# Kernel optimization log

Hardware: AMD Instinct MI355X
Metric: run time of the kernel (lower is better)

Reference implementation:

```python
import jax, jax.numpy as jnp
import numpy as np


def setup_inputs() -> dict:
    key = jax.random.key(0)
    ks = jax.random.split(key, 4)
    B, H, W, C = 4, 64, 64, 256
    d = C // 8
    x = jax.random.normal(ks[0], (B, H, W, C), dtype=jnp.float32)
    # 1x1 conv weights as [C_in, C_out] matrices (Glorot-ish scale)
    Wq = jax.random.normal(ks[1], (C, d), dtype=jnp.float32) * (1.0 / np.sqrt(C))
    Wk = jax.random.normal(ks[2], (C, d), dtype=jnp.float32) * (1.0 / np.sqrt(C))
    Wv = jax.random.normal(ks[3], (C, C), dtype=jnp.float32) * (1.0 / np.sqrt(C))
    bq = jnp.zeros((d,), dtype=jnp.float32)
    bk = jnp.zeros((d,), dtype=jnp.float32)
    bv = jnp.zeros((C,), dtype=jnp.float32)
    gamma = jnp.float32(0.0)  # matches tf.Variable(0.0)
    return {"x": x, "Wq": Wq, "bq": bq, "Wk": Wk, "bk": bk, "Wv": Wv, "bv": bv, "gamma": gamma}


def reference(x, Wq, bq, Wk, bk, Wv, bv, gamma):
    B, H, W, C = x.shape
    N = H * W
    xf = x.reshape(B, N, C)  # spatial tokens
    q = xf @ Wq + bq  # [B, N, d]
    k = xf @ Wk + bk  # [B, N, d]
    v = xf @ Wv + bv  # [B, N, C]
    energy = jnp.einsum("bnd,bmd->bnm", q, k)  # [B, N, N]
    attn = jax.nn.softmax(energy, axis=-1)
    out = jnp.einsum("bnm,bmc->bnc", attn, v).reshape(B, H, W, C)
    return gamma * out + x
```

## Files before the change

kernel.cpp:

```cpp
#include <hip/hip_runtime.h>
#include <hip/hip_bf16.h>

typedef __attribute__((ext_vector_type(8)))  short short8;
typedef __attribute__((ext_vector_type(4)))  float f32x4;
typedef __attribute__((ext_vector_type(16))) float f32x16;
typedef __attribute__((ext_vector_type(4)))  unsigned int u32x4;

#define LOG2E 1.4426950408889634f

static __device__ __forceinline__ unsigned short f2bf(float f) {
    union { float f; unsigned u; } v; v.f = f;
    unsigned r = v.u + 0x7fffu + ((v.u >> 16) & 1u);
    return (unsigned short)(r >> 16);
}
static __device__ __forceinline__ unsigned cvt_pk_bf16(float lo, float hi) {
    unsigned r;
    asm("v_cvt_pk_bf16_f32 %0, %1, %2" : "=v"(r) : "v"(lo), "v"(hi));
    return r;
}
static __device__ __forceinline__ float exp2_hw(float x) {
    float r;
    asm("v_exp_f32 %0, %1" : "=v"(r) : "v"(x));
    return r;
}

__global__ __launch_bounds__(64) void transpose_w(
    const float* __restrict__ Wq, const float* __restrict__ Wk,
    const float* __restrict__ Wv, unsigned short* __restrict__ Wtf)
{
    const int g  = blockIdx.x;
    const int ct = g >> 3, kk = g & 7;
    const int l  = threadIdx.x;
    const int col = ct * 16 + (l & 15);
    const int k0  = kk * 32 + (l >> 4) * 8;
    const float* W; int c, ldw;
    if (col < 32)      { W = Wq; c = col;      ldw = 32;  }
    else if (col < 64) { W = Wk; c = col - 32; ldw = 32;  }
    else               { W = Wv; c = col - 64; ldw = 256; }
    ushort4 o0, o1;
    o0.x = f2bf(W[(size_t)(k0 + 0) * ldw + c]);
    o0.y = f2bf(W[(size_t)(k0 + 1) * ldw + c]);
    o0.z = f2bf(W[(size_t)(k0 + 2) * ldw + c]);
    o0.w = f2bf(W[(size_t)(k0 + 3) * ldw + c]);
    o1.x = f2bf(W[(size_t)(k0 + 4) * ldw + c]);
    o1.y = f2bf(W[(size_t)(k0 + 5) * ldw + c]);
    o1.z = f2bf(W[(size_t)(k0 + 6) * ldw + c]);
    o1.w = f2bf(W[(size_t)(k0 + 7) * ldw + c]);
    *reinterpret_cast<ushort4*>(Wtf + (size_t)g * 512 + l * 8)     = o0;
    *reinterpret_cast<ushort4*>(Wtf + (size_t)g * 512 + l * 8 + 4) = o1;
}

__global__ __launch_bounds__(256) void proj_kernel(
    const float* __restrict__ x, const unsigned short* __restrict__ Wtf,
    const float* __restrict__ bq, const float* __restrict__ bk,
    const float* __restrict__ bv,
    unsigned short* __restrict__ Qb, unsigned short* __restrict__ Kf,
    unsigned short* __restrict__ Vf)
{
    __shared__ unsigned short x_lds[64][264];
    const int tid = threadIdx.x;
    const int M0  = (blockIdx.x >> 1) * 64;
    const int ctb = (blockIdx.x & 1) * 10;

    #pragma unroll
    for (int j = 0; j < 16; ++j) {
        int idx = j * 256 + tid;
        int row = idx >> 6;
        int qc  = idx & 63;
        const float4 v = *reinterpret_cast<const float4*>(x + (size_t)(M0 + row) * 256 + qc * 4);
        ushort4 o;
        o.x = f2bf(v.x); o.y = f2bf(v.y); o.z = f2bf(v.z); o.w = f2bf(v.w);
        *reinterpret_cast<ushort4*>(&x_lds[row][qc * 4]) = o;
    }
    __syncthreads();

    const int w  = tid >> 6;
    const int l  = tid & 63;
    const int lr = l & 15;
    const int lg = l >> 4;

    short8 a[8];
    #pragma unroll
    for (int kk = 0; kk < 8; ++kk)
        a[kk] = *reinterpret_cast<const short8*>(&x_lds[w * 16 + lr][kk * 32 + lg * 8]);

    const int b   = M0 >> 12;
    const int kt  = (M0 & 4095) >> 6;

    for (int ct = ctb; ct < ctb + 10; ++ct) {
        const int col = ct * 16 + lr;
        f32x4 acc = {0.f, 0.f, 0.f, 0.f};
        #pragma unroll
        for (int kk = 0; kk < 8; ++kk) {
            const short8 bfr = *reinterpret_cast<const short8*>(
                Wtf + ((size_t)ct * 8 + kk) * 512 + l * 8);
            acc = __builtin_amdgcn_mfma_f32_16x16x32_bf16(a[kk], bfr, acc, 0, 0, 0);
        }
        const int rbase = M0 + w * 16 + lg * 4;
        if (ct < 2) {
            const float bias = bq[col];
            #pragma unroll
            for (int r = 0; r < 4; ++r)
                Qb[(size_t)(rbase + r) * 32 + col] = f2bf((acc[r] + bias) * LOG2E);
        } else if (ct < 4) {
            const int colp = col - 32;
            const float bias = bk[colp];
            const int dd = colp >> 4, hj = (colp >> 3) & 1, jj = colp & 7;
            #pragma unroll
            for (int r = 0; r < 4; ++r) {
                const int tt = (rbase + r) & 4095;
                const size_t e = (size_t)b * 131072 + (size_t)kt * 2048
                               + (((tt >> 5) & 1) * 2 + dd) * 512
                               + (hj * 32 + (tt & 31)) * 8 + jj;
                Kf[e] = f2bf(acc[r] + bias);
            }
        } else {
            const int colp = col - 64;
            const float bias = bv[colp];
            const int kk_f = w;
            const int hi_v = (lg >> 1) & 1;
            const int j0   = (lg & 1) * 4;
            const size_t e = (size_t)b * 1048576 + (size_t)kt * 16384
                           + (colp >> 5) * 2048 + kk_f * 512
                           + (hi_v * 32 + (colp & 31)) * 8 + j0;
            ushort4 o;
            o.x = f2bf(acc[0] + bias); o.y = f2bf(acc[1] + bias);
            o.z = f2bf(acc[2] + bias); o.w = f2bf(acc[3] + bias);
            *reinterpret_cast<ushort4*>(Vf + e) = o;
        }
    }
}

__global__ __launch_bounds__(512, 2) void attn_kernel(
    const unsigned short* __restrict__ Qb, const unsigned short* __restrict__ Kf,
    const unsigned short* __restrict__ Vf, const float* __restrict__ x,
    const float* __restrict__ gamma_p, float* __restrict__ out)
{
    __shared__ float Obuf[2][32][260];
    __shared__ float lbuf[2][4][32];

    const int i  = blockIdx.x;
    const int b  = i & 3;
    const int qt = i >> 2;

    const int tid = threadIdx.x;
    const int w   = tid >> 6;
    const int qs  = w & 1;
    const int kh  = w >> 1;
    const int l   = tid & 63;
    const int l5  = l & 31;
    const int hi  = l >> 5;

    const size_t bN = (size_t)b * 4096;
    const int q0 = qt * 64;

    const unsigned short* Kfb = Kf + (size_t)b * 131072 + l * 8;
    const unsigned short* Vfb = Vf + (size_t)b * 1048576 + l * 8;

    short8 qb[2];
    #pragma unroll
    for (int dd = 0; dd < 2; ++dd)
        qb[dd] = *reinterpret_cast<const short8*>(
            Qb + (bN + (size_t)(q0 + qs * 32 + l5)) * 32 + dd * 16 + hi * 8);

    f32x16 Oa[8];
    #pragma unroll
    for (int ct = 0; ct < 8; ++ct)
        #pragma unroll
        for (int r = 0; r < 16; ++r) Oa[ct][r] = 0.f;
    float lsum0 = 0.f, lsum1 = 0.f;

    f32x16 z;
    #pragma unroll
    for (int r = 0; r < 16; ++r) z[r] = 0.f;

    const int kt0 = kh * 16;

    auto loadK = [&](short8 (&kA)[2][2], int ktg) {
        const unsigned short* kp = Kfb + (size_t)ktg * 2048;
        #pragma unroll
        for (int ks = 0; ks < 2; ++ks)
            #pragma unroll
            for (int dd = 0; dd < 2; ++dd)
                kA[ks][dd] = *reinterpret_cast<const short8*>(kp + (ks * 2 + dd) * 512);
    };

    short8 pa[4];
    auto build_pa = [&](const f32x16& p, int base) {
        float e[16];
        #pragma unroll
        for (int r = 0; r < 16; ++r) {
            e[r] = exp2_hw(p[r]);
            if (r & 1) lsum1 += e[r]; else lsum0 += e[r];
        }
        unsigned c[8];
        #pragma unroll
        for (int n = 0; n < 8; ++n) c[n] = cvt_pk_bf16(e[2 * n], e[2 * n + 1]);
        #pragma unroll
        for (int k2 = 0; k2 < 2; ++k2) {
            unsigned d0 = c[4 * k2 + 0], d2 = c[4 * k2 + 2];
            unsigned d1 = c[4 * k2 + 1], d3 = c[4 * k2 + 3];
            asm("v_permlane32_swap_b32 %0, %1" : "+v"(d0), "+v"(d2));
            asm("v_permlane32_swap_b32 %0, %1" : "+v"(d1), "+v"(d3));
            u32x4 u = {d0, d1, d2, d3};
            pa[base + k2] = __builtin_bit_cast(short8, u);
        }
    };

    auto body = [&](short8 (&kcur)[2][2], short8 (&knxt)[2][2], int ktg, int ktgn) {
        const unsigned short* vp = Vfb + (size_t)ktg * 16384;
        short8 vf[2][4];
        #pragma unroll
        for (int kk = 0; kk < 4; ++kk)
            vf[0][kk] = *reinterpret_cast<const short8*>(vp + kk * 512);
        loadK(knxt, ktgn);
        {
            f32x16 p = __builtin_amdgcn_mfma_f32_32x32x16_bf16(kcur[0][0], qb[0], z, 0, 0, 0);
            p        = __builtin_amdgcn_mfma_f32_32x32x16_bf16(kcur[0][1], qb[1], p, 0, 0, 0);
            build_pa(p, 0);
        }
        {
            f32x16 p = __builtin_amdgcn_mfma_f32_32x32x16_bf16(kcur[1][0], qb[0], z, 0, 0, 0);
            p        = __builtin_amdgcn_mfma_f32_32x32x16_bf16(kcur[1][1], qb[1], p, 0, 0, 0);
            build_pa(p, 2);
        }
        __builtin_amdgcn_s_setprio(1);
        #pragma unroll
        for (int ct = 0; ct < 8; ++ct) {
            if (ct < 7) {
                #pragma unroll
                for (int kk = 0; kk < 4; ++kk)
                    vf[(ct + 1) & 1][kk] = *reinterpret_cast<const short8*>(
                        vp + (ct + 1) * 2048 + kk * 512);
            }
            #pragma unroll
            for (int kk = 0; kk < 4; ++kk)
                Oa[ct] = __builtin_amdgcn_mfma_f32_32x32x16_bf16(pa[kk], vf[ct & 1][kk], Oa[ct], 0, 0, 0);
        }
        __builtin_amdgcn_s_setprio(0);
    };

    short8 kA0[2][2], kA1[2][2];
    loadK(kA0, kt0);
    for (int kt = 0; kt < 16; kt += 2) {
        body(kA0, kA1, kt0 + kt, kt0 + kt + 1);
        body(kA1, kA0, kt0 + kt + 1, kt0 + ((kt + 2) & 15));
    }

    lsum0 += lsum1;
    lsum0 += __shfl_xor(lsum0, 32);
    if (hi == 0) lbuf[qs][kh][l5] = lsum0;

    for (int s = 0; s < 4; ++s) {
        if (kh == s) {
            #pragma unroll
            for (int ct = 0; ct < 8; ++ct)
                #pragma unroll
                for (int r = 0; r < 16; ++r) {
                    const int qr = (r & 3) + 8 * (r >> 2) + 4 * hi;
                    float* p = &Obuf[qs][qr][ct * 32 + l5];
                    if (s == 0) *p = Oa[ct][r]; else *p += Oa[ct][r];
                }
        }
        __syncthreads();
    }

    const float gamma = gamma_p[0];
    const int er  = w * 8 + (l >> 3);
    const int eqs = er >> 5, eq = er & 31;
    const float ltot = lbuf[eqs][0][eq] + lbuf[eqs][1][eq]
                     + lbuf[eqs][2][eq] + lbuf[eqs][3][eq];
    const float linv = gamma / ltot;
    #pragma unroll
    for (int it = 0; it < 8; ++it) {
        const int c4 = (l & 7) + it * 8;
        const f32x4 o = *reinterpret_cast<const f32x4*>(&Obuf[eqs][eq][c4 * 4]);
        const size_t idx = (bN + (size_t)(q0 + er)) * 256 + c4 * 4;
        const float4 xi = *reinterpret_cast<const float4*>(x + idx);
        float4 ov;
        ov.x = o[0] * linv + xi.x;
        ov.y = o[1] * linv + xi.y;
        ov.z = o[2] * linv + xi.z;
        ov.w = o[3] * linv + xi.w;
        *reinterpret_cast<float4*>(out + idx) = ov;
    }
}

extern "C" void kernel_launch(void* const* d_in, const int* in_sizes, int n_in,
                              void* d_out, int out_size, void* d_ws, size_t ws_size,
                              hipStream_t stream) {
    const float* x     = (const float*)d_in[0];
    const float* Wq    = (const float*)d_in[1];
    const float* bq    = (const float*)d_in[2];
    const float* Wk    = (const float*)d_in[3];
    const float* bk    = (const float*)d_in[4];
    const float* Wv    = (const float*)d_in[5];
    const float* bv    = (const float*)d_in[6];
    const float* gamma = (const float*)d_in[7];
    float* out = (float*)d_out;

    unsigned short* Qb  = (unsigned short*)d_ws;
    unsigned short* Kf  = Qb + (size_t)16384 * 32;
    unsigned short* Vf  = Kf + (size_t)16384 * 32;
    unsigned short* Wtf = Vf + (size_t)4 * 256 * 4096;

    transpose_w<<<160, 64, 0, stream>>>(Wq, Wk, Wv, Wtf);
    proj_kernel<<<512, 256, 0, stream>>>(x, Wtf, bq, bk, bv, Qb, Kf, Vf);
    attn_kernel<<<256, 512, 0, stream>>>(Qb, Kf, Vf, x, gamma, out);
}
```

Measured before the change: 98.79 us.

## Repartition attention into small blocks with column split and MFMA row sums

Splits attention work differently: each 128-thread block handles 32 queries and half of the value channels, with two waves splitting the keys, launched as 1024 blocks instead of 256 blocks of 512 threads. Softmax row sums are now computed with an MFMA against a ones vector rather than scalar adds, and the cross-wave reduction uses a single shared-memory exchange. Each block loads all four column tiles of V up front. The aim is better CU occupancy and less VALU and LDS reduction work, at the cost of recomputing QK^T and exp twice per query (once per column group) and holding more V registers.

```diff
diff --git a/kernel.cpp b/kernel.cpp
--- a/kernel.cpp
+++ b/kernel.cpp
@@ -131,50 +131,57 @@
     }
 }
 
-__global__ __launch_bounds__(512, 2) void attn_kernel(
+__global__ __launch_bounds__(128, 2) void attn_kernel(
     const unsigned short* __restrict__ Qb, const unsigned short* __restrict__ Kf,
     const unsigned short* __restrict__ Vf, const float* __restrict__ x,
     const float* __restrict__ gamma_p, float* __restrict__ out)
 {
-    __shared__ float Obuf[2][32][260];
-    __shared__ float lbuf[2][4][32];
+    __shared__ float O_sh[4][16][64];
+    __shared__ float l_sh[2][32];
 
     const int i  = blockIdx.x;
-    const int b  = i & 3;
-    const int qt = i >> 2;
+    const int b  = (i & 7) >> 1;
+    const int t  = ((i >> 3) << 1) | (i & 1);
+    const int qt = t >> 1;
+    const int cg = t & 1;
 
     const int tid = threadIdx.x;
-    const int w   = tid >> 6;
-    const int qs  = w & 1;
-    const int kh  = w >> 1;
+    const int kh  = tid >> 6;
     const int l   = tid & 63;
     const int l5  = l & 31;
     const int hi  = l >> 5;
 
     const size_t bN = (size_t)b * 4096;
-    const int q0 = qt * 64;
+    const int q0 = qt * 32;
+    const int c0 = cg * 128;
 
     const unsigned short* Kfb = Kf + (size_t)b * 131072 + l * 8;
-    const unsigned short* Vfb = Vf + (size_t)b * 1048576 + l * 8;
+    const unsigned short* Vfb = Vf + (size_t)b * 1048576 + (c0 >> 5) * 2048 + l * 8;
 
     short8 qb[2];
     #pragma unroll
     for (int dd = 0; dd < 2; ++dd)
         qb[dd] = *reinterpret_cast<const short8*>(
-            Qb + (bN + (size_t)(q0 + qs * 32 + l5)) * 32 + dd * 16 + hi * 8);
-
-    f32x16 Oa[8];
-    #pragma unroll
-    for (int ct = 0; ct < 8; ++ct)
+            Qb + (bN + (size_t)(q0 + l5)) * 32 + dd * 16 + hi * 8);
+
+    short8 onesB;
+    #pragma unroll
+    for (int j = 0; j < 8; ++j) onesB[j] = (short)0x3F80;
+
+    f32x16 Oa[4];
+    #pragma unroll
+    for (int ct = 0; ct < 4; ++ct)
         #pragma unroll
         for (int r = 0; r < 16; ++r) Oa[ct][r] = 0.f;
-    float lsum0 = 0.f, lsum1 = 0.f;
+    f32x16 Os;
+    #pragma unroll
+    for (int r = 0; r < 16; ++r) Os[r] = 0.f;
 
     f32x16 z;
     #pragma unroll
     for (int r = 0; r < 16; ++r) z[r] = 0.f;
 
-    const int kt0 = kh * 16;
+    const int kt0 = kh * 32;
 
     auto loadK = [&](short8 (&kA)[2][2], int ktg) {
         const unsigned short* kp = Kfb + (size_t)ktg * 2048;
@@ -187,15 +194,10 @@
 
     short8 pa[4];
     auto build_pa = [&](const f32x16& p, int base) {
-        float e[16];
-        #pragma unroll
-        for (int r = 0; r < 16; ++r) {
-            e[r] = exp2_hw(p[r]);
-            if (r & 1) lsum1 += e[r]; else lsum0 += e[r];
-        }
         unsigned c[8];
         #pragma unroll
-        for (int n = 0; n < 8; ++n) c[n] = cvt_pk_bf16(e[2 * n], e[2 * n + 1]);
+        for (int n = 0; n < 8; ++n)
+            c[n] = cvt_pk_bf16(exp2_hw(p[2 * n]), exp2_hw(p[2 * n + 1]));
         #pragma unroll
         for (int k2 = 0; k2 < 2; ++k2) {
             unsigned d0 = c[4 * k2 + 0], d2 = c[4 * k2 + 2];
@@ -209,10 +211,12 @@
 
     auto body = [&](short8 (&kcur)[2][2], short8 (&knxt)[2][2], int ktg, int ktgn) {
         const unsigned short* vp = Vfb + (size_t)ktg * 16384;
-        short8 vf[2][4];
-        #pragma unroll
-        for (int kk = 0; kk < 4; ++kk)
-            vf[0][kk] = *reinterpret_cast<const short8*>(vp + kk * 512);
+        short8 vf[4][4];
+        #pragma unroll
+        for (int ct = 0; ct < 4; ++ct)
+            #pragma unroll
+            for (int kk = 0; kk < 4; ++kk)
+                vf[ct][kk] = *reinterpret_cast<const short8*>(vp + ct * 2048 + kk * 512);
         loadK(knxt, ktgn);
         {
             f32x16 p = __builtin_amdgcn_mfma_f32_32x32x16_bf16(kcur[0][0], qb[0], z, 0, 0, 0);
@@ -224,66 +228,52 @@
             p        = __builtin_amdgcn_mfma_f32_32x32x16_bf16(kcur[1][1], qb[1], p, 0, 0, 0);
             build_pa(p, 2);
         }
+        #pragma unroll
+        for (int kk = 0; kk < 4; ++kk)
+            Os = __builtin_amdgcn_mfma_f32_32x32x16_bf16(pa[kk], onesB, Os, 0, 0, 0);
         __builtin_amdgcn_s_setprio(1);
         #pragma unroll
-        for (int ct = 0; ct < 8; ++ct) {
-            if (ct < 7) {
-                #pragma unroll
-                for (int kk = 0; kk < 4; ++kk)
-                    vf[(ct + 1) & 1][kk] = *reinterpret_cast<const short8*>(
-                        vp + (ct + 1) * 2048 + kk * 512);
-            }
+        for (int ct = 0; ct < 4; ++ct)
             #pragma unroll
             for (int kk = 0; kk < 4; ++kk)
-                Oa[ct] = __builtin_amdgcn_mfma_f32_32x32x16_bf16(pa[kk], vf[ct & 1][kk], Oa[ct], 0, 0, 0);
-        }
+                Oa[ct] = __builtin_amdgcn_mfma_f32_32x32x16_bf16(pa[kk], vf[ct][kk], Oa[ct], 0, 0, 0);
         __builtin_amdgcn_s_setprio(0);
     };
 
     short8 kA0[2][2], kA1[2][2];
     loadK(kA0, kt0);
-    for (int kt = 0; kt < 16; kt += 2) {
+    for (int kt = 0; kt < 32; kt += 2) {
         body(kA0, kA1, kt0 + kt, kt0 + kt + 1);
-        body(kA1, kA0, kt0 + kt + 1, kt0 + ((kt + 2) & 15));
+        body(kA1, kA0, kt0 + kt + 1, kt0 + ((kt + 2) & 31));
     }
 
-    lsum0 += lsum1;
-    lsum0 += __shfl_xor(lsum0, 32);
-    if (hi == 0) lbuf[qs][kh][l5] = lsum0;
-
-    for (int s = 0; s < 4; ++s) {
-        if (kh == s) {
-            #pragma unroll
-            for (int ct = 0; ct < 8; ++ct)
-                #pragma unroll
-                for (int r = 0; r < 16; ++r) {
-                    const int qr = (r & 3) + 8 * (r >> 2) + 4 * hi;
-                    float* p = &Obuf[qs][qr][ct * 32 + l5];
-                    if (s == 0) *p = Oa[ct][r]; else *p += Oa[ct][r];
-                }
-        }
-        __syncthreads();
+    if (l5 == 0) {
+        #pragma unroll
+        for (int r = 0; r < 16; ++r)
+            l_sh[kh][(r & 3) + 8 * (r >> 2) + 4 * hi] = Os[r];
     }
+    #pragma unroll
+    for (int ct = 0; ct < 4; ++ct)
+        if ((ct >> 1) != kh) {
+            #pragma unroll
+            for (int r = 0; r < 16; ++r)
+                O_sh[ct][r][hi * 32 + l5] = Oa[ct][r];
+        }
+    __syncthreads();
 
     const float gamma = gamma_p[0];
-    const int er  = w * 8 + (l >> 3);
-    const int eqs = er >> 5, eq = er & 31;
-    const float ltot = lbuf[eqs][0][eq] + lbuf[eqs][1][eq]
-                     + lbuf[eqs][2][eq] + lbuf[eqs][3][eq];
-    const float linv = gamma / ltot;
-    #pragma unroll
-    for (int it = 0; it < 8; ++it) {
-        const int c4 = (l & 7) + it * 8;
-        const f32x4 o = *reinterpret_cast<const f32x4*>(&Obuf[eqs][eq][c4 * 4]);
-        const size_t idx = (bN + (size_t)(q0 + er)) * 256 + c4 * 4;
-        const float4 xi = *reinterpret_cast<const float4*>(x + idx);
-        float4 ov;
-        ov.x = o[0] * linv + xi.x;
-        ov.y = o[1] * linv + xi.y;
-        ov.z = o[2] * linv + xi.z;
-        ov.w = o[3] * linv + xi.w;
-        *reinterpret_cast<float4*>(out + idx) = ov;
-    }
+    #pragma unroll
+    for (int ct = 0; ct < 4; ++ct)
+        if ((ct >> 1) == kh) {
+            #pragma unroll
+            for (int r = 0; r < 16; ++r) {
+                const int qr = (r & 3) + 8 * (r >> 2) + 4 * hi;
+                const float ltot = l_sh[0][qr] + l_sh[1][qr];
+                const float osum = Oa[ct][r] + O_sh[ct][r][hi * 32 + l5];
+                const size_t idx = (bN + (size_t)(q0 + qr)) * 256 + c0 + ct * 32 + l5;
+                out[idx] = gamma * (osum / ltot) + x[idx];
+            }
+        }
 }
 
 extern "C" void kernel_launch(void* const* d_in, const int* in_sizes, int n_in,
@@ -306,5 +296,5 @@
 
     transpose_w<<<160, 64, 0, stream>>>(Wq, Wk, Wv, Wtf);
     proj_kernel<<<512, 256, 0, stream>>>(x, Wtf, bq, bk, bv, Qb, Kf, Vf);
-    attn_kernel<<<256, 512, 0, stream>>>(Qb, Kf, Vf, x, gamma, out);
-}
+    attn_kernel<<<1024, 128, 0, stream>>>(Qb, Kf, Vf, x, gamma, out);
+}
```

New measurement: 88.47 us. 10.4% less time.
